# Kernel tuning notes

Measured on AMD Instinct MI355X. Metric: run time of the kernel, lower is better.

## Reference

```python
import jax, jax.numpy as jnp
import numpy as np

B, N, DIM = 4, 8192, 1024
HEADS, DIM_HEAD = 16, 64


def setup_inputs() -> dict:
    key = jax.random.key(0)
    ks = jax.random.split(key, 6)
    s = 1.0 / np.sqrt(DIM_HEAD)
    so = 1.0 / np.sqrt(HEADS * DIM_HEAD)
    return {
        "x": jax.random.normal(ks[0], (B, N, DIM), dtype=jnp.float32),
        "Wq": jax.random.uniform(ks[1], (DIM_HEAD, DIM_HEAD), jnp.float32, -s, s),
        "Wk": jax.random.uniform(ks[2], (DIM_HEAD, DIM_HEAD), jnp.float32, -s, s),
        "Wv": jax.random.uniform(ks[3], (DIM_HEAD, DIM_HEAD), jnp.float32, -s, s),
        "Wo": jax.random.uniform(ks[4], (DIM, HEADS * DIM_HEAD), jnp.float32, -so, so),
        "bo": jax.random.uniform(ks[5], (DIM,), jnp.float32, -so, so),
    }


def reference(x, Wq, Wk, Wv, Wo, bo):
    Bs, Ns, Cs = x.shape
    # [B, H, N, Dh]
    xh = x.reshape(Bs, Ns, HEADS, DIM_HEAD).transpose(0, 2, 1, 3)
    # torch Linear: y = x @ W.T
    q = jnp.einsum('bhnd,ed->bhne', xh, Wq)
    k = jnp.einsum('bhnd,ed->bhne', xh, Wk)
    v = jnp.einsum('bhnd,ed->bhne', xh, Wv)
    # k^T v: [B, H, Dh, Dh], normalized by N (dropout is identity, p=0)
    dots = jnp.einsum('bhnd,bhne->bhde', k, v) / float(Ns)
    res = jnp.einsum('bhnd,bhde->bhne', q, dots)
    # b h n d -> b n (h d)
    res = res.transpose(0, 2, 1, 3).reshape(Bs, Ns, HEADS * DIM_HEAD)
    return res @ Wo.T + bo
```

## Files before the change

### kernel.cpp

```cpp
#include <hip/hip_runtime.h>

#define DIMC 1024
#define NSEQ 8192
#define DH 64

typedef __attribute__((ext_vector_type(8))) short short8;
typedef __attribute__((ext_vector_type(4))) float f32x4;

__device__ __forceinline__ short f2bf(float f) {
  union { float f; unsigned u; } v; v.f = f;
  unsigned r = v.u + 0x7FFFu + ((v.u >> 16) & 1u);
  return (short)(r >> 16);
}

__device__ __forceinline__ unsigned pack_bf2(float a, float b) {
  union { float f; unsigned u; } va, vb;
  va.f = a; vb.f = b;
  unsigned ua = va.u + 0x8000u;
  unsigned ub = vb.u + 0x8000u;
  return (ua >> 16) | (ub & 0xFFFF0000u);
}

__device__ __forceinline__ unsigned bfbits(float f) {
  union { float f; unsigned u; } v; v.f = f;
  return (v.u + 0x8000u) >> 16;
}
__device__ __forceinline__ float bf2f(unsigned hb) {
  union { unsigned u; float f; } v; v.u = hb << 16;
  return v.f;
}

__device__ __forceinline__ void gload_lds16(const void* g, void* l) {
  __builtin_amdgcn_global_load_lds(
      (const __attribute__((address_space(1))) void*)g,
      (__attribute__((address_space(3))) void*)l, 16, 0, 0);
}

__global__ __launch_bounds__(256) void gram2_kernel(const float* __restrict__ x,
                                                    float* __restrict__ Gpart,
                                                    short* __restrict__ xbf) {
  int chunk = blockIdx.x, bh = blockIdx.y;
  int b = bh >> 4, h = bh & 15;
  int t = threadIdx.x;
  int w = t >> 6, l = t & 63;
  int quad = l >> 4, ln = l & 15;

  __shared__ __align__(16) short XT[4][2][64 * 32];
  __shared__ __align__(16) float Pred[3][4096];
  short* XH = &XT[w][0][0];
  short* XL = &XT[w][1][0];

  size_t rowbase = (size_t)b * NSEQ + (size_t)chunk * 1024 + w * 256;
  const float* xb = x + rowbase * DIMC + h * DH;
  short* xo = xbf + rowbase * DIMC + h * DH;

  f32x4 acc[4][4];
#pragma unroll
  for (int i = 0; i < 4; i++)
#pragma unroll
    for (int j = 0; j < 4; j++) acc[i][j] = (f32x4){0.f, 0.f, 0.f, 0.f};

  int woff[4][4];
#pragma unroll
  for (int q = 0; q < 4; q++) {
    int kk = 8 * q + 2 * quad;
    int kp = kk ^ ((ln & 3) << 3);
#pragma unroll
    for (int i = 0; i < 4; i++) {
      int d = ln * 4 + i;
      woff[q][i] = d * 32 + kp;
    }
  }
  int roff[4];
  {
    int k0 = (quad * 8) ^ ((ln >> 2) << 3);
#pragma unroll
    for (int i = 0; i < 4; i++) roff[i] = (i * 16 + ln) * 32 + k0;
  }

  float4 cur[4][2];
#pragma unroll
  for (int q = 0; q < 4; q++)
#pragma unroll
    for (int r = 0; r < 2; r++)
      cur[q][r] = *(const float4*)(xb + (size_t)(8 * q + 2 * quad + r) * DIMC + ln * 4);

  for (int ks = 0; ks < 8; ks++) {
    float4 nxt[4][2];
    if (ks < 7) {
      int nb = (ks + 1) * 32;
#pragma unroll
      for (int q = 0; q < 4; q++)
#pragma unroll
        for (int r = 0; r < 2; r++)
          nxt[q][r] = *(const float4*)(xb + (size_t)(nb + 8 * q + 2 * quad + r) * DIMC + ln * 4);
    }
#pragma unroll
    for (int q = 0; q < 4; q++) {
      unsigned h0[4], h1[4], l0[4], l1[4];
#pragma unroll
      for (int i = 0; i < 4; i++) {
        float a = cur[q][0][i], bb = cur[q][1][i];
        h0[i] = bfbits(a); l0[i] = bfbits(a - bf2f(h0[i]));
        h1[i] = bfbits(bb); l1[i] = bfbits(bb - bf2f(h1[i]));
      }
      int grow = ks * 32 + 8 * q + 2 * quad;
      uint2 p0 = {h0[0] | (h0[1] << 16), h0[2] | (h0[3] << 16)};
      uint2 p1 = {h1[0] | (h1[1] << 16), h1[2] | (h1[3] << 16)};
      *(uint2*)(xo + (size_t)grow * DIMC + ln * 4) = p0;
      *(uint2*)(xo + (size_t)(grow + 1) * DIMC + ln * 4) = p1;
#pragma unroll
      for (int i = 0; i < 4; i++) {
        *(unsigned*)&XH[woff[q][i]] = h0[i] | (h1[i] << 16);
        *(unsigned*)&XL[woff[q][i]] = l0[i] | (l1[i] << 16);
      }
    }
    short8 hf[4], lf[4];
#pragma unroll
    for (int i = 0; i < 4; i++) {
      hf[i] = *(const short8*)&XH[roff[i]];
      lf[i] = *(const short8*)&XL[roff[i]];
    }
#pragma unroll
    for (int i = 0; i < 4; i++)
#pragma unroll
      for (int j = 0; j < 4; j++) {
        acc[i][j] = __builtin_amdgcn_mfma_f32_16x16x32_bf16(hf[i], hf[j], acc[i][j], 0, 0, 0);
        acc[i][j] = __builtin_amdgcn_mfma_f32_16x16x32_bf16(hf[i], lf[j], acc[i][j], 0, 0, 0);
        acc[i][j] = __builtin_amdgcn_mfma_f32_16x16x32_bf16(lf[i], hf[j], acc[i][j], 0, 0, 0);
      }
#pragma unroll
    for (int q = 0; q < 4; q++)
#pragma unroll
      for (int r = 0; r < 2; r++) cur[q][r] = nxt[q][r];
  }

  if (w > 0) {
    float* pd = &Pred[w - 1][0];
#pragma unroll
    for (int i = 0; i < 4; i++)
#pragma unroll
      for (int j = 0; j < 4; j++)
#pragma unroll
        for (int r = 0; r < 4; r++) {
          int d = i * 16 + quad * 4 + r, e = j * 16 + ln;
          pd[d * 64 + e] = acc[i][j][r];
        }
  }
  __syncthreads();
  if (w == 0) {
    float* gp = Gpart + (size_t)chunk * (64 * 4096) + (size_t)bh * 4096;
#pragma unroll
    for (int i = 0; i < 4; i++)
#pragma unroll
      for (int j = 0; j < 4; j++)
#pragma unroll
        for (int r = 0; r < 4; r++) {
          int d = i * 16 + quad * 4 + r, e = j * 16 + ln;
          int idx = d * 64 + e;
          gp[idx] = acc[i][j][r] + Pred[0][idx] + Pred[1][idx] + Pred[2][idx];
        }
  }
}

__global__ __launch_bounds__(64) void gram_kernel(const float* __restrict__ x,
                                                  float* __restrict__ Gpart,
                                                  short* __restrict__ xbf) {
  int chunk = blockIdx.x, bh = blockIdx.y;
  int b = bh >> 4, h = bh & 15;
  int t = threadIdx.x;
  __shared__ __align__(16) float rows[16 * 64];
  const float* xb = x + ((size_t)b * NSEQ) * DIMC + h * DH;
  short* xo = xbf ? xbf + ((size_t)b * NSEQ) * DIMC + h * DH : (short*)0;
  int d0 = (t >> 3) * 8, e0 = (t & 7) * 8;
  float acc[8][8] = {};
  float4 v[4];
#pragma unroll
  for (int i = 0; i < 4; i++) {
    int f4 = i * 64 + t;
    v[i] = *(const float4*)(xb + (size_t)(chunk * 256 + (f4 >> 4)) * DIMC + (f4 & 15) * 4);
  }
  for (int it = 0; it < 16; it++) {
    __syncthreads();
#pragma unroll
    for (int i = 0; i < 4; i++) ((float4*)rows)[i * 64 + t] = v[i];
    __syncthreads();
    if (xo) {
#pragma unroll
      for (int i = 0; i < 4; i++) {
        int f4 = i * 64 + t;
        int row = chunk * 256 + it * 16 + (f4 >> 4), col = (f4 & 15) * 4;
        uint2 pw = {pack_bf2(v[i].x, v[i].y), pack_bf2(v[i].z, v[i].w)};
        *(uint2*)(xo + (size_t)row * DIMC + col) = pw;
      }
    }
    if (it < 15) {
      int nbase = chunk * 256 + (it + 1) * 16;
#pragma unroll
      for (int i = 0; i < 4; i++) {
        int f4 = i * 64 + t;
        v[i] = *(const float4*)(xb + (size_t)(nbase + (f4 >> 4)) * DIMC + (f4 & 15) * 4);
      }
    }
#pragma unroll
    for (int r = 0; r < 16; r++) {
      float xd[8], xe[8];
      *(float4*)&xd[0] = *(const float4*)&rows[r * 64 + d0];
      *(float4*)&xd[4] = *(const float4*)&rows[r * 64 + d0 + 4];
      *(float4*)&xe[0] = *(const float4*)&rows[r * 64 + e0];
      *(float4*)&xe[4] = *(const float4*)&rows[r * 64 + e0 + 4];
#pragma unroll
      for (int i = 0; i < 8; i++)
#pragma unroll
        for (int j = 0; j < 8; j++) acc[i][j] = fmaf(xd[i], xe[j], acc[i][j]);
    }
  }
  float* gp = Gpart + (size_t)chunk * (64 * 4096) + (size_t)bh * 4096;
#pragma unroll
  for (int i = 0; i < 8; i++)
#pragma unroll
    for (int j = 0; j < 8; j++) gp[(d0 + i) * 64 + e0 + j] = acc[i][j];
}

__global__ void reduce_g(const float* __restrict__ Gpart, float* __restrict__ G,
                         int np) {
  int i = blockIdx.x * 256 + threadIdx.x;
  float s = 0.f;
  for (int p = 0; p < np; p++) s += Gpart[(size_t)p * (64 * 4096) + i];
  G[i] = s;
}

__global__ __launch_bounds__(256) void combine8_kernel(
    const float* __restrict__ Gpart, const float* __restrict__ Wq,
    const float* __restrict__ Wk, const float* __restrict__ Wv,
    const float* __restrict__ Wo, short* __restrict__ WbigT) {
  int bh = blockIdx.x, qt = blockIdx.y;
  int b = bh >> 4, h = bh & 15;
  int t = threadIdx.x;
  __shared__ __align__(16) float sG[4096];
  __shared__ __align__(16) float sW[4096];
  __shared__ __align__(16) float sA[4096];
  __shared__ __align__(16) float sM[4096];

  for (int i = t; i < 4096; i += 256) {
    float s = 0.f;
#pragma unroll
    for (int p = 0; p < 8; p++)
      s += Gpart[(size_t)p * (64 * 4096) + (size_t)bh * 4096 + i];
    sG[i] = s;
  }
  for (int i = t; i < 4096; i += 256) sW[i] = Wk[i];
  __syncthreads();

  int d0 = (t >> 4) * 4, e0 = (t & 15) * 4;
  {
    float a[4][4] = {};
    for (int fg = 0; fg < 16; fg++) {
      float wk[4][4], g4[4][4];
#pragma unroll
      for (int i = 0; i < 4; i++) *(float4*)wk[i] = *(const float4*)&sW[(d0 + i) * 64 + fg * 4];
#pragma unroll
      for (int ff = 0; ff < 4; ff++) *(float4*)g4[ff] = *(const float4*)&sG[(fg * 4 + ff) * 64 + e0];
#pragma unroll
      for (int i = 0; i < 4; i++)
#pragma unroll
        for (int ff = 0; ff < 4; ff++)
#pragma unroll
          for (int j = 0; j < 4; j++) a[i][j] = fmaf(wk[i][ff], g4[ff][j], a[i][j]);
    }
#pragma unroll
    for (int i = 0; i < 4; i++)
#pragma unroll
      for (int j = 0; j < 4; j++) sA[(d0 + i) * 64 + e0 + j] = a[i][j];
  }
  __syncthreads();
  for (int i = t; i < 4096; i += 256) sW[i] = Wv[i];
  __syncthreads();
  {
    float a[4][4] = {};
    for (int fgi = 0; fgi < 16; fgi++) {
      int fg = (fgi + (t & 15)) & 15;
      float t1[4][4], wv[4][4];
#pragma unroll
      for (int i = 0; i < 4; i++) *(float4*)t1[i] = *(const float4*)&sA[(d0 + i) * 64 + fg * 4];
#pragma unroll
      for (int j = 0; j < 4; j++) *(float4*)wv[j] = *(const float4*)&sW[(e0 + j) * 64 + fg * 4];
#pragma unroll
      for (int i = 0; i < 4; i++)
#pragma unroll
        for (int j = 0; j < 4; j++)
#pragma unroll
          for (int ff = 0; ff < 4; ff++) a[i][j] = fmaf(t1[i][ff], wv[j][ff], a[i][j]);
    }
    __syncthreads();
#pragma unroll
    for (int i = 0; i < 4; i++)
#pragma unroll
      for (int j = 0; j < 4; j++) sG[(d0 + i) * 64 + e0 + j] = a[i][j];
  }
  __syncthreads();
  for (int i = t; i < 4096; i += 256) sW[i] = Wq[i];
  __syncthreads();
  {
    float a[4][4] = {};
    for (int f = 0; f < 64; f++) {
      float wq[4], t2[4];
      *(float4*)wq = *(const float4*)&sW[f * 64 + d0];
      *(float4*)t2 = *(const float4*)&sG[f * 64 + e0];
#pragma unroll
      for (int i = 0; i < 4; i++)
#pragma unroll
        for (int j = 0; j < 4; j++) a[i][j] = fmaf(wq[i], t2[j], a[i][j]);
    }
#pragma unroll
    for (int i = 0; i < 4; i++)
#pragma unroll
      for (int j = 0; j < 4; j++) sM[(d0 + i) * 64 + e0 + j] = a[i][j] * (1.0f / 8192.0f);
  }
  __syncthreads();
  int dd0 = (t & 15) * 4, cl0 = (t >> 4) * 4;
  for (int cc = qt * 2; cc < qt * 2 + 2; cc++) {
    int c0 = cc * 64;
    for (int i = t; i < 4096; i += 256)
      sW[i] = Wo[(size_t)(c0 + (i >> 6)) * DIMC + h * DH + (i & 63)];
    __syncthreads();
    float a[4][4] = {};
    for (int egi = 0; egi < 16; egi++) {
      int eg = (egi + (t & 15)) & 15;
      float m4[4][4], wo4[4][4];
#pragma unroll
      for (int i = 0; i < 4; i++) *(float4*)m4[i] = *(const float4*)&sM[(dd0 + i) * 64 + eg * 4];
#pragma unroll
      for (int j = 0; j < 4; j++) *(float4*)wo4[j] = *(const float4*)&sW[(cl0 + j) * 64 + eg * 4];
#pragma unroll
      for (int i = 0; i < 4; i++)
#pragma unroll
        for (int j = 0; j < 4; j++)
#pragma unroll
          for (int ff = 0; ff < 4; ff++) a[i][j] = fmaf(m4[i][ff], wo4[j][ff], a[i][j]);
    }
#pragma unroll
    for (int j = 0; j < 4; j++) {
      uint2 pw = {pack_bf2(a[0][j], a[1][j]), pack_bf2(a[2][j], a[3][j])};
      *(uint2*)&WbigT[((size_t)b << 20) + (size_t)(c0 + cl0 + j) * DIMC + h * DH + dd0] = pw;
    }
    __syncthreads();
  }
}

__global__ __launch_bounds__(256) void combine_kernel(
    const float* __restrict__ G, const float* __restrict__ Wq,
    const float* __restrict__ Wk, const float* __restrict__ Wv,
    const float* __restrict__ Wo, short* __restrict__ WbigT) {
  int bh = blockIdx.x, qt = blockIdx.y;
  int b = bh >> 4, h = bh & 15;
  int t = threadIdx.x;
  __shared__ __align__(16) float sG[4096];
  __shared__ __align__(16) float sW[4096];
  __shared__ __align__(16) float sA[4096];
  __shared__ __align__(16) float sM[4096];

  for (int i = t; i < 4096; i += 256) sG[i] = G[(size_t)bh * 4096 + i];
  for (int i = t; i < 4096; i += 256) sW[i] = Wk[i];
  __syncthreads();

  int d0 = (t >> 4) * 4, e0 = (t & 15) * 4;
  {
    float a[4][4] = {};
    for (int fg = 0; fg < 16; fg++) {
      float wk[4][4], g4[4][4];
#pragma unroll
      for (int i = 0; i < 4; i++) *(float4*)wk[i] = *(const float4*)&sW[(d0 + i) * 64 + fg * 4];
#pragma unroll
      for (int ff = 0; ff < 4; ff++) *(float4*)g4[ff] = *(const float4*)&sG[(fg * 4 + ff) * 64 + e0];
#pragma unroll
      for (int i = 0; i < 4; i++)
#pragma unroll
        for (int ff = 0; ff < 4; ff++)
#pragma unroll
          for (int j = 0; j < 4; j++) a[i][j] = fmaf(wk[i][ff], g4[ff][j], a[i][j]);
    }
#pragma unroll
    for (int i = 0; i < 4; i++)
#pragma unroll
      for (int j = 0; j < 4; j++) sA[(d0 + i) * 64 + e0 + j] = a[i][j];
  }
  __syncthreads();
  for (int i = t; i < 4096; i += 256) sW[i] = Wv[i];
  __syncthreads();
  {
    float a[4][4] = {};
    for (int fgi = 0; fgi < 16; fgi++) {
      int fg = (fgi + (t & 15)) & 15;
      float t1[4][4], wv[4][4];
#pragma unroll
      for (int i = 0; i < 4; i++) *(float4*)t1[i] = *(const float4*)&sA[(d0 + i) * 64 + fg * 4];
#pragma unroll
      for (int j = 0; j < 4; j++) *(float4*)wv[j] = *(const float4*)&sW[(e0 + j) * 64 + fg * 4];
#pragma unroll
      for (int i = 0; i < 4; i++)
#pragma unroll
        for (int j = 0; j < 4; j++)
#pragma unroll
          for (int ff = 0; ff < 4; ff++) a[i][j] = fmaf(t1[i][ff], wv[j][ff], a[i][j]);
    }
    __syncthreads();
#pragma unroll
    for (int i = 0; i < 4; i++)
#pragma unroll
      for (int j = 0; j < 4; j++) sG[(d0 + i) * 64 + e0 + j] = a[i][j];
  }
  __syncthreads();
  for (int i = t; i < 4096; i += 256) sW[i] = Wq[i];
  __syncthreads();
  {
    float a[4][4] = {};
    for (int f = 0; f < 64; f++) {
      float wq[4], t2[4];
      *(float4*)wq = *(const float4*)&sW[f * 64 + d0];
      *(float4*)t2 = *(const float4*)&sG[f * 64 + e0];
#pragma unroll
      for (int i = 0; i < 4; i++)
#pragma unroll
        for (int j = 0; j < 4; j++) a[i][j] = fmaf(wq[i], t2[j], a[i][j]);
    }
#pragma unroll
    for (int i = 0; i < 4; i++)
#pragma unroll
      for (int j = 0; j < 4; j++) sM[(d0 + i) * 64 + e0 + j] = a[i][j] * (1.0f / 8192.0f);
  }
  __syncthreads();
  int dd0 = (t & 15) * 4, cl0 = (t >> 4) * 4;
  for (int cc = qt * 2; cc < qt * 2 + 2; cc++) {
    int c0 = cc * 64;
    for (int i = t; i < 4096; i += 256)
      sW[i] = Wo[(size_t)(c0 + (i >> 6)) * DIMC + h * DH + (i & 63)];
    __syncthreads();
    float a[4][4] = {};
    for (int egi = 0; egi < 16; egi++) {
      int eg = (egi + (t & 15)) & 15;
      float m4[4][4], wo4[4][4];
#pragma unroll
      for (int i = 0; i < 4; i++) *(float4*)m4[i] = *(const float4*)&sM[(dd0 + i) * 64 + eg * 4];
#pragma unroll
      for (int j = 0; j < 4; j++) *(float4*)wo4[j] = *(const float4*)&sW[(cl0 + j) * 64 + eg * 4];
#pragma unroll
      for (int i = 0; i < 4; i++)
#pragma unroll
        for (int j = 0; j < 4; j++)
#pragma unroll
          for (int ff = 0; ff < 4; ff++) a[i][j] = fmaf(m4[i][ff], wo4[j][ff], a[i][j]);
    }
#pragma unroll
    for (int j = 0; j < 4; j++) {
      uint2 pw = {pack_bf2(a[0][j], a[1][j]), pack_bf2(a[2][j], a[3][j])};
      *(uint2*)&WbigT[((size_t)b << 20) + (size_t)(c0 + cl0 + j) * DIMC + h * DH + dd0] = pw;
    }
    __syncthreads();
  }
}

__global__ __launch_bounds__(256, 3) void gemm_small(
    const float* __restrict__ x, const short* __restrict__ WbigT,
    const float* __restrict__ bo, float* __restrict__ out) {
  int bid = blockIdx.x;
  int xcd = bid & 7, r = bid >> 3;
  int g = r >> 5, q = r & 31;
  int m_blk = g * 32 + xcd * 4 + (q >> 3);
  int n_blk = q & 7;
  int b = m_blk >> 6;
  int row0 = m_blk * 128;
  int c0 = n_blk * 128;

  __shared__ __align__(16) short As[128 * 32];
  __shared__ __align__(16) short Bs[128 * 32];

  int t = threadIdx.x;
  int lane = t & 63, wave = t >> 6;
  int wm = wave >> 1, wn = wave & 1;
  int quad = lane >> 4, ln = lane & 15;

  f32x4 acc[4][4];
#pragma unroll
  for (int i = 0; i < 4; i++)
#pragma unroll
    for (int j = 0; j < 4; j++) acc[i][j] = (f32x4){0.f, 0.f, 0.f, 0.f};

  const short* Bbase = WbigT + ((size_t)b << 20);

  int e_base[2], crow_[2], lc_[2];
#pragma unroll
  for (int L = 0; L < 2; L++) {
    int e = (wave * 2 + L) * 512 + lane * 8;
    e_base[L] = e;
    int crow = e >> 5;
    crow_[L] = crow;
    lc_[L] = ((e >> 3) & 3) ^ ((crow >> 1) & 3);
  }

  for (int kt = 0; kt < 32; kt++) {
    int k0 = kt * 32;
    __syncthreads();
#pragma unroll
    for (int L = 0; L < 2; L++)
      gload_lds16(Bbase + (size_t)(c0 + crow_[L]) * DIMC + k0 + lc_[L] * 8, &Bs[e_base[L]]);
#pragma unroll
    for (int qq = 0; qq < 2; qq++) {
      int elem = qq * 2048 + wave * 512 + lane * 8;
      int m = elem >> 5, kk = elem & 31;
      const float* gp = x + (size_t)(row0 + m) * DIMC + k0 + kk;
      float4 v0 = *(const float4*)gp;
      float4 v1 = *(const float4*)(gp + 4);
      unsigned w0 = pack_bf2(v0.x, v0.y), w1 = pack_bf2(v0.z, v0.w);
      unsigned w2 = pack_bf2(v1.x, v1.y), w3 = pack_bf2(v1.z, v1.w);
      unsigned tmp[4] = {w0, w1, w2, w3};
      int pe = ((elem >> 3) & 3) ^ ((m >> 1) & 3);
      *(short8*)&As[m * 32 + pe * 8] = *(short8*)tmp;
    }
    __syncthreads();
    short8 afrag[4], bfrag[4];
#pragma unroll
    for (int i = 0; i < 4; i++) {
      int ar = wm * 64 + i * 16 + ln;
      afrag[i] = *(const short8*)&As[ar * 32 + (quad ^ ((ar >> 1) & 3)) * 8];
      int br = wn * 64 + i * 16 + ln;
      bfrag[i] = *(const short8*)&Bs[br * 32 + (quad ^ ((br >> 1) & 3)) * 8];
    }
#pragma unroll
    for (int i = 0; i < 4; i++)
#pragma unroll
      for (int j = 0; j < 4; j++)
        acc[i][j] = __builtin_amdgcn_mfma_f32_16x16x32_bf16(afrag[i], bfrag[j], acc[i][j], 0, 0, 0);
  }

  float bov[4];
#pragma unroll
  for (int j = 0; j < 4; j++) bov[j] = bo[c0 + wn * 64 + j * 16 + ln];
#pragma unroll
  for (int i = 0; i < 4; i++)
#pragma unroll
    for (int j = 0; j < 4; j++) {
      int col = c0 + wn * 64 + j * 16 + ln;
#pragma unroll
      for (int rr = 0; rr < 4; rr++) {
        int row = row0 + wm * 64 + i * 16 + quad * 4 + rr;
        out[(size_t)row * DIMC + col] = acc[i][j][rr] + bov[j];
      }
    }
}

__global__ __launch_bounds__(256, 3) void gemm_big(
    const short* __restrict__ xbf, const short* __restrict__ WbigT,
    const float* __restrict__ bo, float* __restrict__ out) {
  int bid = blockIdx.x;
  int xcd = bid & 7, r = bid >> 3;
  int g = r >> 5, q = r & 31;
  int m_blk = g * 32 + xcd * 4 + (q >> 3);
  int n_blk = q & 7;
  int b = m_blk >> 6;
  int row0 = m_blk * 128;
  int c0 = n_blk * 128;

  __shared__ __align__(16) short As[128 * 32];
  __shared__ __align__(16) short Bs[128 * 32];

  int t = threadIdx.x;
  int lane = t & 63, wave = t >> 6;
  int wm = wave >> 1, wn = wave & 1;
  int quad = lane >> 4, ln = lane & 15;

  f32x4 acc[4][4];
#pragma unroll
  for (int i = 0; i < 4; i++)
#pragma unroll
    for (int j = 0; j < 4; j++) acc[i][j] = (f32x4){0.f, 0.f, 0.f, 0.f};

  const short* Bbase = WbigT + ((size_t)b << 20);

  int e_base[2];
  const short* Asrc[2];
  const short* Bsrc[2];
#pragma unroll
  for (int L = 0; L < 2; L++) {
    int e = (wave * 2 + L) * 512 + lane * 8;
    e_base[L] = e;
    int row = e >> 5;
    int lc = ((e >> 3) & 3) ^ ((row >> 1) & 3);
    Asrc[L] = xbf + (size_t)(row0 + row) * DIMC + lc * 8;
    Bsrc[L] = Bbase + (size_t)(c0 + row) * DIMC + lc * 8;
  }

  for (int kt = 0; kt < 32; kt++) {
    int k0 = kt * 32;
    __syncthreads();
#pragma unroll
    for (int L = 0; L < 2; L++) gload_lds16(Asrc[L] + k0, &As[e_base[L]]);
#pragma unroll
    for (int L = 0; L < 2; L++) gload_lds16(Bsrc[L] + k0, &Bs[e_base[L]]);
    __syncthreads();
    short8 afrag[4], bfrag[4];
#pragma unroll
    for (int i = 0; i < 4; i++) {
      int ar = wm * 64 + i * 16 + ln;
      afrag[i] = *(const short8*)&As[ar * 32 + (quad ^ ((ar >> 1) & 3)) * 8];
      int br = wn * 64 + i * 16 + ln;
      bfrag[i] = *(const short8*)&Bs[br * 32 + (quad ^ ((br >> 1) & 3)) * 8];
    }
#pragma unroll
    for (int i = 0; i < 4; i++)
#pragma unroll
      for (int j = 0; j < 4; j++)
        acc[i][j] = __builtin_amdgcn_mfma_f32_16x16x32_bf16(afrag[i], bfrag[j], acc[i][j], 0, 0, 0);
  }

  float bov[4];
#pragma unroll
  for (int j = 0; j < 4; j++) bov[j] = bo[c0 + wn * 64 + j * 16 + ln];
#pragma unroll
  for (int i = 0; i < 4; i++)
#pragma unroll
    for (int j = 0; j < 4; j++) {
      int col = c0 + wn * 64 + j * 16 + ln;
#pragma unroll
      for (int rr = 0; rr < 4; rr++) {
        int row = row0 + wm * 64 + i * 16 + quad * 4 + rr;
        out[(size_t)row * DIMC + col] = acc[i][j][rr] + bov[j];
      }
    }
}

extern "C" void kernel_launch(void* const* d_in, const int* in_sizes, int n_in,
                              void* d_out, int out_size, void* d_ws, size_t ws_size,
                              hipStream_t stream) {
  const float* x  = (const float*)d_in[0];
  const float* Wq = (const float*)d_in[1];
  const float* Wk = (const float*)d_in[2];
  const float* Wv = (const float*)d_in[3];
  const float* Wo = (const float*)d_in[4];
  const float* bo = (const float*)d_in[5];
  float* out = (float*)d_out;
  (void)in_sizes; (void)n_in; (void)out_size;

  if (ws_size >= ((size_t)81 << 20)) {
    short* xbf   = (short*)d_ws;
    float* Gpart = (float*)((char*)d_ws + ((size_t)64 << 20));
    short* WbigT = (short*)((char*)d_ws + ((size_t)72 << 20));
    gram2_kernel<<<dim3(8, 64), 256, 0, stream>>>(x, Gpart, xbf);
    combine8_kernel<<<dim3(64, 8), 256, 0, stream>>>(Gpart, Wq, Wk, Wv, Wo, WbigT);
    gemm_big<<<2048, 256, 0, stream>>>(xbf, WbigT, bo, out);
  } else {
    float* Gpart = (float*)d_ws;
    float* G     = (float*)((char*)d_ws + ((size_t)32 << 20));
    short* WbigT = (short*)((char*)d_ws + ((size_t)33 << 20));
    gram_kernel<<<dim3(32, 64), 64, 0, stream>>>(x, Gpart, (short*)0);
    reduce_g<<<1024, 256, 0, stream>>>(Gpart, G, 32);
    combine_kernel<<<dim3(64, 8), 256, 0, stream>>>(G, Wq, Wk, Wv, Wo, WbigT);
    gemm_small<<<2048, 256, 0, stream>>>(x, WbigT, bo, out);
  }
}
```

Before: 365.5 us.

## Widen GEMM K-tile to 64, precompute Wq^T·Wk, split reduction from combine

The main bf16 GEMM now stages a K-tile of 64 instead of 32, which halves the number of barrier pairs. It uses an 8-way XOR swizzle and issues two MFMAs per fragment pair per stage. The per-(b,h) combine no longer reduces the Gram partials or multiplies by Wq. A separate reduce kernel sums the partials and also computes P = Wq^T·Wk once. The combine kernel then does only P·G, then ·Wv, then ·Wo. This adds a kernel launch and a round trip of G through memory, and the larger shared tiles may reduce occupancy.

```diff
diff --git a/kernel.cpp b/kernel.cpp
--- a/kernel.cpp
+++ b/kernel.cpp
@@ -230,35 +230,63 @@
   G[i] = s;
 }
 
-__global__ __launch_bounds__(256) void combine8_kernel(
-    const float* __restrict__ Gpart, const float* __restrict__ Wq,
-    const float* __restrict__ Wk, const float* __restrict__ Wv,
-    const float* __restrict__ Wo, short* __restrict__ WbigT) {
+__global__ __launch_bounds__(256) void reduce_gp(
+    const float* __restrict__ Gpart, float* __restrict__ G, int np,
+    const float* __restrict__ Wq, const float* __restrict__ Wk,
+    float* __restrict__ P) {
+  __shared__ __align__(16) float sq[4096];
+  __shared__ __align__(16) float sk[4096];
+  int i = blockIdx.x * 256 + threadIdx.x;
+  float s = 0.f;
+  for (int p = 0; p < np; p++) s += Gpart[(size_t)p * (64 * 4096) + i];
+  G[i] = s;
+  if (blockIdx.x == 0) {
+    int t = threadIdx.x;
+    for (int j = t; j < 4096; j += 256) { sq[j] = Wq[j]; sk[j] = Wk[j]; }
+    __syncthreads();
+    int d0 = (t >> 4) * 4, e0 = (t & 15) * 4;
+    float a[4][4] = {};
+    for (int f = 0; f < 64; f++) {
+      float q4[4], k4[4];
+      *(float4*)q4 = *(const float4*)&sq[f * 64 + d0];
+      *(float4*)k4 = *(const float4*)&sk[f * 64 + e0];
+#pragma unroll
+      for (int ii = 0; ii < 4; ii++)
+#pragma unroll
+        for (int jj = 0; jj < 4; jj++) a[ii][jj] = fmaf(q4[ii], k4[jj], a[ii][jj]);
+    }
+#pragma unroll
+    for (int ii = 0; ii < 4; ii++)
+#pragma unroll
+      for (int jj = 0; jj < 4; jj++) P[(d0 + ii) * 64 + e0 + jj] = a[ii][jj];
+  }
+}
+
+__global__ __launch_bounds__(256) void combine_p(
+    const float* __restrict__ G, const float* __restrict__ P,
+    const float* __restrict__ Wv, const float* __restrict__ Wo,
+    short* __restrict__ WbigT) {
   int bh = blockIdx.x, qt = blockIdx.y;
   int b = bh >> 4, h = bh & 15;
   int t = threadIdx.x;
   __shared__ __align__(16) float sG[4096];
-  __shared__ __align__(16) float sW[4096];
-  __shared__ __align__(16) float sA[4096];
+  __shared__ __align__(16) float sP[4096];
+  __shared__ __align__(16) float sV[4096];
+  __shared__ __align__(16) float sT[4096];
   __shared__ __align__(16) float sM[4096];
 
-  for (int i = t; i < 4096; i += 256) {
-    float s = 0.f;
-#pragma unroll
-    for (int p = 0; p < 8; p++)
-      s += Gpart[(size_t)p * (64 * 4096) + (size_t)bh * 4096 + i];
-    sG[i] = s;
-  }
-  for (int i = t; i < 4096; i += 256) sW[i] = Wk[i];
+  for (int i = t; i < 4096; i += 256) sG[i] = G[(size_t)bh * 4096 + i];
+  for (int i = t; i < 4096; i += 256) sP[i] = P[i];
+  for (int i = t; i < 4096; i += 256) sV[i] = Wv[i];
   __syncthreads();
 
   int d0 = (t >> 4) * 4, e0 = (t & 15) * 4;
   {
     float a[4][4] = {};
     for (int fg = 0; fg < 16; fg++) {
-      float wk[4][4], g4[4][4];
-#pragma unroll
-      for (int i = 0; i < 4; i++) *(float4*)wk[i] = *(const float4*)&sW[(d0 + i) * 64 + fg * 4];
+      float pk[4][4], g4[4][4];
+#pragma unroll
+      for (int i = 0; i < 4; i++) *(float4*)pk[i] = *(const float4*)&sP[(d0 + i) * 64 + fg * 4];
 #pragma unroll
       for (int ff = 0; ff < 4; ff++) *(float4*)g4[ff] = *(const float4*)&sG[(fg * 4 + ff) * 64 + e0];
 #pragma unroll
@@ -266,15 +294,13 @@
 #pragma unroll
         for (int ff = 0; ff < 4; ff++)
 #pragma unroll
-          for (int j = 0; j < 4; j++) a[i][j] = fmaf(wk[i][ff], g4[ff][j], a[i][j]);
-    }
-#pragma unroll
-    for (int i = 0; i < 4; i++)
-#pragma unroll
-      for (int j = 0; j < 4; j++) sA[(d0 + i) * 64 + e0 + j] = a[i][j];
-  }
-  __syncthreads();
-  for (int i = t; i < 4096; i += 256) sW[i] = Wv[i];
+          for (int j = 0; j < 4; j++) a[i][j] = fmaf(pk[i][ff], g4[ff][j], a[i][j]);
+    }
+#pragma unroll
+    for (int i = 0; i < 4; i++)
+#pragma unroll
+      for (int j = 0; j < 4; j++) sT[(d0 + i) * 64 + e0 + j] = a[i][j];
+  }
   __syncthreads();
   {
     float a[4][4] = {};
@@ -282,35 +308,15 @@
       int fg = (fgi + (t & 15)) & 15;
       float t1[4][4], wv[4][4];
 #pragma unroll
-      for (int i = 0; i < 4; i++) *(float4*)t1[i] = *(const float4*)&sA[(d0 + i) * 64 + fg * 4];
-#pragma unroll
-      for (int j = 0; j < 4; j++) *(float4*)wv[j] = *(const float4*)&sW[(e0 + j) * 64 + fg * 4];
+      for (int i = 0; i < 4; i++) *(float4*)t1[i] = *(const float4*)&sT[(d0 + i) * 64 + fg * 4];
+#pragma unroll
+      for (int j = 0; j < 4; j++) *(float4*)wv[j] = *(const float4*)&sV[(e0 + j) * 64 + fg * 4];
 #pragma unroll
       for (int i = 0; i < 4; i++)
 #pragma unroll
         for (int j = 0; j < 4; j++)
 #pragma unroll
           for (int ff = 0; ff < 4; ff++) a[i][j] = fmaf(t1[i][ff], wv[j][ff], a[i][j]);
-    }
-    __syncthreads();
-#pragma unroll
-    for (int i = 0; i < 4; i++)
-#pragma unroll
-      for (int j = 0; j < 4; j++) sG[(d0 + i) * 64 + e0 + j] = a[i][j];
-  }
-  __syncthreads();
-  for (int i = t; i < 4096; i += 256) sW[i] = Wq[i];
-  __syncthreads();
-  {
-    float a[4][4] = {};
-    for (int f = 0; f < 64; f++) {
-      float wq[4], t2[4];
-      *(float4*)wq = *(const float4*)&sW[f * 64 + d0];
-      *(float4*)t2 = *(const float4*)&sG[f * 64 + e0];
-#pragma unroll
-      for (int i = 0; i < 4; i++)
-#pragma unroll
-        for (int j = 0; j < 4; j++) a[i][j] = fmaf(wq[i], t2[j], a[i][j]);
     }
 #pragma unroll
     for (int i = 0; i < 4; i++)
@@ -322,7 +328,7 @@
   for (int cc = qt * 2; cc < qt * 2 + 2; cc++) {
     int c0 = cc * 64;
     for (int i = t; i < 4096; i += 256)
-      sW[i] = Wo[(size_t)(c0 + (i >> 6)) * DIMC + h * DH + (i & 63)];
+      sP[i] = Wo[(size_t)(c0 + (i >> 6)) * DIMC + h * DH + (i & 63)];
     __syncthreads();
     float a[4][4] = {};
     for (int egi = 0; egi < 16; egi++) {
@@ -331,7 +337,7 @@
 #pragma unroll
       for (int i = 0; i < 4; i++) *(float4*)m4[i] = *(const float4*)&sM[(dd0 + i) * 64 + eg * 4];
 #pragma unroll
-      for (int j = 0; j < 4; j++) *(float4*)wo4[j] = *(const float4*)&sW[(cl0 + j) * 64 + eg * 4];
+      for (int j = 0; j < 4; j++) *(float4*)wo4[j] = *(const float4*)&sP[(cl0 + j) * 64 + eg * 4];
 #pragma unroll
       for (int i = 0; i < 4; i++)
 #pragma unroll
@@ -549,7 +555,7 @@
     }
 }
 
-__global__ __launch_bounds__(256, 3) void gemm_big(
+__global__ __launch_bounds__(256, 3) void gemm_big64(
     const short* __restrict__ xbf, const short* __restrict__ WbigT,
     const float* __restrict__ bo, float* __restrict__ out) {
   int bid = blockIdx.x;
@@ -561,8 +567,8 @@
   int row0 = m_blk * 128;
   int c0 = n_blk * 128;
 
-  __shared__ __align__(16) short As[128 * 32];
-  __shared__ __align__(16) short Bs[128 * 32];
+  __shared__ __align__(16) short As[128 * 64];
+  __shared__ __align__(16) short Bs[128 * 64];
 
   int t = threadIdx.x;
   int lane = t & 63, wave = t >> 6;
@@ -577,40 +583,46 @@
 
   const short* Bbase = WbigT + ((size_t)b << 20);
 
-  int e_base[2];
-  const short* Asrc[2];
-  const short* Bsrc[2];
-#pragma unroll
-  for (int L = 0; L < 2; L++) {
-    int e = (wave * 2 + L) * 512 + lane * 8;
-    e_base[L] = e;
-    int row = e >> 5;
-    int lc = ((e >> 3) & 3) ^ ((row >> 1) & 3);
-    Asrc[L] = xbf + (size_t)(row0 + row) * DIMC + lc * 8;
-    Bsrc[L] = Bbase + (size_t)(c0 + row) * DIMC + lc * 8;
-  }
-
-  for (int kt = 0; kt < 32; kt++) {
-    int k0 = kt * 32;
-    __syncthreads();
-#pragma unroll
-    for (int L = 0; L < 2; L++) gload_lds16(Asrc[L] + k0, &As[e_base[L]]);
-#pragma unroll
-    for (int L = 0; L < 2; L++) gload_lds16(Bsrc[L] + k0, &Bs[e_base[L]]);
-    __syncthreads();
-    short8 afrag[4], bfrag[4];
+  const short* Asrc[4];
+  const short* Bsrc[4];
+  int doff[4];
+#pragma unroll
+  for (int s = 0; s < 4; s++) {
+    int p = s * 256 + t;
+    int row = p >> 3;
+    int cl = (p & 7) ^ (row & 7);
+    doff[s] = p * 8;
+    Asrc[s] = xbf + (size_t)(row0 + row) * DIMC + cl * 8;
+    Bsrc[s] = Bbase + (size_t)(c0 + row) * DIMC + cl * 8;
+  }
+
+  for (int kt = 0; kt < 16; kt++) {
+    int k0 = kt * 64;
+    __syncthreads();
+#pragma unroll
+    for (int s = 0; s < 4; s++) gload_lds16(Asrc[s] + k0, &As[doff[s]]);
+#pragma unroll
+    for (int s = 0; s < 4; s++) gload_lds16(Bsrc[s] + k0, &Bs[doff[s]]);
+    __syncthreads();
+    short8 af[4][2], bf4[4][2];
 #pragma unroll
     for (int i = 0; i < 4; i++) {
       int ar = wm * 64 + i * 16 + ln;
-      afrag[i] = *(const short8*)&As[ar * 32 + (quad ^ ((ar >> 1) & 3)) * 8];
+#pragma unroll
+      for (int kk = 0; kk < 2; kk++)
+        af[i][kk] = *(const short8*)&As[ar * 64 + (((kk * 4 + quad) ^ (ar & 7)) << 3)];
       int br = wn * 64 + i * 16 + ln;
-      bfrag[i] = *(const short8*)&Bs[br * 32 + (quad ^ ((br >> 1) & 3)) * 8];
+#pragma unroll
+      for (int kk = 0; kk < 2; kk++)
+        bf4[i][kk] = *(const short8*)&Bs[br * 64 + (((kk * 4 + quad) ^ (br & 7)) << 3)];
     }
 #pragma unroll
     for (int i = 0; i < 4; i++)
 #pragma unroll
       for (int j = 0; j < 4; j++)
-        acc[i][j] = __builtin_amdgcn_mfma_f32_16x16x32_bf16(afrag[i], bfrag[j], acc[i][j], 0, 0, 0);
+#pragma unroll
+        for (int kk = 0; kk < 2; kk++)
+          acc[i][j] = __builtin_amdgcn_mfma_f32_16x16x32_bf16(af[i][kk], bf4[j][kk], acc[i][j], 0, 0, 0);
   }
 
   float bov[4];
@@ -641,13 +653,16 @@
   float* out = (float*)d_out;
   (void)in_sizes; (void)n_in; (void)out_size;
 
-  if (ws_size >= ((size_t)81 << 20)) {
+  if (ws_size >= ((size_t)83 << 20)) {
     short* xbf   = (short*)d_ws;
     float* Gpart = (float*)((char*)d_ws + ((size_t)64 << 20));
-    short* WbigT = (short*)((char*)d_ws + ((size_t)72 << 20));
+    float* G     = (float*)((char*)d_ws + ((size_t)72 << 20));
+    float* P     = (float*)((char*)d_ws + ((size_t)73 << 20));
+    short* WbigT = (short*)((char*)d_ws + ((size_t)74 << 20));
     gram2_kernel<<<dim3(8, 64), 256, 0, stream>>>(x, Gpart, xbf);
-    combine8_kernel<<<dim3(64, 8), 256, 0, stream>>>(Gpart, Wq, Wk, Wv, Wo, WbigT);
-    gemm_big<<<2048, 256, 0, stream>>>(xbf, WbigT, bo, out);
+    reduce_gp<<<1024, 256, 0, stream>>>(Gpart, G, 8, Wq, Wk, P);
+    combine_p<<<dim3(64, 8), 256, 0, stream>>>(G, P, Wv, Wo, WbigT);
+    gemm_big64<<<2048, 256, 0, stream>>>(xbf, WbigT, bo, out);
   } else {
     float* Gpart = (float*)d_ws;
     float* G     = (float*)((char*)d_ws + ((size_t)32 << 20));
```

New measurement: 354.1 us. -3.1%, faster.
